# Performance work log

Measured on AMD Instinct MI355X. Metric: run time of the kernel, lower is better.

Reference implementation:

```python
import jax, jax.numpy as jnp
import numpy as np

N, E, IN_DIM, HID, OUT = 50000, 800000, 128, 128, 64


def setup_inputs() -> dict:
    key = jax.random.key(0)
    k = jax.random.split(key, 6)
    h = jax.random.normal(k[0], (N, IN_DIM), dtype=jnp.float32)
    edge_index = jax.random.randint(k[1], (2, E), 0, N, dtype=jnp.int64)
    s_in, s_hid = 1.0 / np.sqrt(IN_DIM), 1.0 / np.sqrt(HID)
    W_gcn = jax.random.uniform(k[2], (IN_DIM, HID), jnp.float32, -s_in, s_in)
    b_gcn = jnp.zeros((HID,), jnp.float32)
    W_fc = jax.random.uniform(k[3], (HID, OUT), jnp.float32, -s_hid, s_hid)
    b_fc = jax.random.uniform(k[4], (OUT,), jnp.float32, -s_hid, s_hid)
    return {"h": h, "edge_index": edge_index, "W_gcn": W_gcn,
            "b_gcn": b_gcn, "W_fc": W_fc, "b_fc": b_fc}


def reference(h, edge_index, W_gcn, b_gcn, W_fc, b_fc):
    n = h.shape[0]
    # GCNConv: transform, add self-loops, symmetric normalization, scatter-add
    x = h @ W_gcn                                   # [N, HID]
    loop = jnp.arange(n, dtype=edge_index.dtype)
    row = jnp.concatenate([edge_index[0], loop])    # source nodes
    col = jnp.concatenate([edge_index[1], loop])    # destination nodes
    deg = jax.ops.segment_sum(jnp.ones_like(col, dtype=x.dtype), col,
                              num_segments=n)       # in-degree incl. self-loop
    dinv = jnp.where(deg > 0, jax.lax.rsqrt(deg), 0.0)
    norm = dinv[row] * dinv[col]                    # [E+N]
    msg = x[row] * norm[:, None]                    # gather + scale
    agg = jax.ops.segment_sum(msg, col, num_segments=n) + b_gcn
    # ReLU then projection
    return jax.nn.relu(agg) @ W_fc + b_fc
```

## Files before the change

kernel.cpp:

```cpp
#include <hip/hip_runtime.h>

#define N_NODES 50000
#define N_EDGES 800000
#define TOT (N_EDGES + N_NODES)
#define NBKT 196
#define BCAP 6144

typedef __attribute__((ext_vector_type(4))) float floatx4;
typedef __attribute__((ext_vector_type(8))) _Float16 half8;
typedef __attribute__((ext_vector_type(2))) _Float16 half2v;

#define O_PTR   0UL
#define O_GF    200192UL
#define O_DINV  201472UL
#define O_ESRC  401664UL
#define O_W1    3801856UL
#define O_W2    3834624UL
#define O_U     3851008UL
#define O_H16   16651008UL

__global__ __launch_bounds__(256) void k_binA(const int* __restrict__ ei,
                                              int* __restrict__ gfill,
                                              unsigned* __restrict__ staging) {
    __shared__ int cnt[NBKT];
    __shared__ int gbase[NBKT];
    __shared__ int s_i64;
    int t = threadIdx.x;
    if (t < 64) {
        unsigned w = ((const unsigned*)ei)[2 * t + 1];
        unsigned long long m = __ballot(w == 0u);
        if (t == 0) s_i64 = (__popcll(m) >= 60) ? 1 : 0;
    }
    for (int i = t; i < NBKT; i += 256) cnt[i] = 0;
    __syncthreads();
    bool i64 = s_i64 != 0;
    int ebase = blockIdx.x * 4096;
    unsigned pk[16]; int rk[16]; short bk[16];
#pragma unroll
    for (int j = 0; j < 16; ++j) {
        int e = ebase + j * 256 + t;
        if (e < N_EDGES) {
            int s, d;
            if (i64) { s = ei[2 * e]; d = ei[2 * (N_EDGES + e)]; }
            else     { s = ei[e];     d = ei[N_EDGES + e]; }
            int b = d >> 8;
            bk[j] = (short)b;
            pk[j] = (unsigned)s | ((unsigned)(d & 255) << 16);
            rk[j] = atomicAdd(&cnt[b], 1);
        } else bk[j] = -1;
    }
    __syncthreads();
    for (int i = t; i < NBKT; i += 256)
        gbase[i] = atomicAdd(&gfill[i], cnt[i]);
    __syncthreads();
#pragma unroll
    for (int j = 0; j < 16; ++j) {
        if (bk[j] >= 0) {
            int pos = gbase[bk[j]] + rk[j];
            if (pos < BCAP) staging[(size_t)bk[j] * BCAP + pos] = pk[j];
        }
    }
}

__global__ __launch_bounds__(256) void k_binB(const unsigned* __restrict__ staging,
                                              const int* __restrict__ gfill,
                                              const float* __restrict__ h,
                                              const float* __restrict__ Wg,
                                              const float* __restrict__ Wf,
                                              int* __restrict__ ptr,
                                              float* __restrict__ dinv,
                                              _Float16* __restrict__ h16,
                                              _Float16* __restrict__ W1,
                                              _Float16* __restrict__ W2,
                                              int* __restrict__ esrc) {
    __shared__ unsigned se[BCAP];
    __shared__ int lcnt[256];
    __shared__ int lscan[256];
    __shared__ int cur[256];
    __shared__ float sdinv[256];
    __shared__ int s_cb;
    int b = blockIdx.x, t = threadIdx.x;
    if (b < 64) {
        int i = b * 256 + t;
        int n = i >> 7, k = i & 127;
        W1[i] = (_Float16)Wg[k * 128 + n];
    } else if (b < 96) {
        int i = (b - 64) * 256 + t;
        int n = i >> 7, k = i & 127;
        W2[i] = (_Float16)Wf[k * 64 + n];
    }
    int nbase = b * 256;
    int nn = min(256, N_NODES - nbase);
    int cnt = min(gfill[b], BCAP);
    if (t < 64) {
        int acc = 0;
        for (int i = t; i < b; i += 64) acc += min(gfill[i], BCAP) + 256;
#pragma unroll
        for (int off = 32; off > 0; off >>= 1) acc += __shfl_down(acc, off);
        if (t == 0) s_cb = acc;
    }
    lcnt[t] = 0;
    __syncthreads();
    int cb = s_cb;
    const unsigned* st = staging + (size_t)b * BCAP;
    for (int i = t; i < cnt; i += 256) {
        unsigned p = st[i];
        se[i] = p;
        atomicAdd(&lcnt[p >> 16], 1);
    }
    __syncthreads();
    int v = lcnt[t];
    lscan[t] = v;
    __syncthreads();
    for (int off = 1; off < 256; off <<= 1) {
        int x = (t >= off) ? lscan[t - off] : 0;
        __syncthreads(); lscan[t] += x; __syncthreads();
    }
    int segstart = cb + (lscan[t] - v) + t;
    float dv = rsqrtf((float)(v + 1));
    if (t < nn) {
        int node = nbase + t;
        ptr[node] = segstart;
        dinv[node] = dv;
        sdinv[t] = dv;
        esrc[segstart] = node;
        cur[t] = segstart + 1;
    }
    __syncthreads();
    for (int i = t; i < cnt; i += 256) {
        unsigned p = se[i];
        int pos = atomicAdd(&cur[p >> 16], 1);
        esrc[pos] = (int)(p & 0xffffu);
    }
    int half = t >> 7;
    int col = t & 127;
    for (int r = half; r < nn; r += 2) {
        int node = nbase + r;
        h16[(size_t)node * 128 + col] = (_Float16)(h[(size_t)node * 128 + col] * sdinv[r]);
    }
}

__global__ __launch_bounds__(256) void k_agg(const _Float16* __restrict__ h16,
                                             const int* __restrict__ ptr,
                                             const int* __restrict__ esrc,
                                             const float* __restrict__ dinv,
                                             _Float16* __restrict__ u) {
    int wid = (blockIdx.x * 256 + threadIdx.x) >> 6;
    int lane = threadIdx.x & 63;
    if (wid >= N_NODES) return;
    int p0 = ptr[wid];
    int p1 = (wid + 1 < N_NODES) ? ptr[wid + 1] : TOT;
    float a0 = 0.f, a1 = 0.f;
    for (int base = p0; base < p1; base += 64) {
        int cnt = p1 - base; if (cnt > 64) cnt = 64;
        int idx = 0;
        if (lane < cnt) idx = esrc[base + lane];
        int j = 0;
        for (; j + 8 <= cnt; j += 8) {
            int s0 = __shfl(idx, j),     s1 = __shfl(idx, j + 1);
            int s2 = __shfl(idx, j + 2), s3 = __shfl(idx, j + 3);
            int s4 = __shfl(idx, j + 4), s5 = __shfl(idx, j + 5);
            int s6 = __shfl(idx, j + 6), s7 = __shfl(idx, j + 7);
            half2v u0 = *(const half2v*)(h16 + (size_t)s0 * 128 + lane * 2);
            half2v u1 = *(const half2v*)(h16 + (size_t)s1 * 128 + lane * 2);
            half2v u2 = *(const half2v*)(h16 + (size_t)s2 * 128 + lane * 2);
            half2v u3 = *(const half2v*)(h16 + (size_t)s3 * 128 + lane * 2);
            half2v u4 = *(const half2v*)(h16 + (size_t)s4 * 128 + lane * 2);
            half2v u5 = *(const half2v*)(h16 + (size_t)s5 * 128 + lane * 2);
            half2v u6 = *(const half2v*)(h16 + (size_t)s6 * 128 + lane * 2);
            half2v u7 = *(const half2v*)(h16 + (size_t)s7 * 128 + lane * 2);
            a0 += (float)u0[0] + (float)u1[0] + (float)u2[0] + (float)u3[0]
                + (float)u4[0] + (float)u5[0] + (float)u6[0] + (float)u7[0];
            a1 += (float)u0[1] + (float)u1[1] + (float)u2[1] + (float)u3[1]
                + (float)u4[1] + (float)u5[1] + (float)u6[1] + (float)u7[1];
        }
        for (; j + 4 <= cnt; j += 4) {
            int s0 = __shfl(idx, j),     s1 = __shfl(idx, j + 1);
            int s2 = __shfl(idx, j + 2), s3 = __shfl(idx, j + 3);
            half2v u0 = *(const half2v*)(h16 + (size_t)s0 * 128 + lane * 2);
            half2v u1 = *(const half2v*)(h16 + (size_t)s1 * 128 + lane * 2);
            half2v u2 = *(const half2v*)(h16 + (size_t)s2 * 128 + lane * 2);
            half2v u3 = *(const half2v*)(h16 + (size_t)s3 * 128 + lane * 2);
            a0 += (float)u0[0] + (float)u1[0] + (float)u2[0] + (float)u3[0];
            a1 += (float)u0[1] + (float)u1[1] + (float)u2[1] + (float)u3[1];
        }
        for (; j < cnt; ++j) {
            int s = __shfl(idx, j);
            half2v uu = *(const half2v*)(h16 + (size_t)s * 128 + lane * 2);
            a0 += (float)uu[0]; a1 += (float)uu[1];
        }
    }
    float sc = dinv[wid];
    half2v o; o[0] = (_Float16)(a0 * sc); o[1] = (_Float16)(a1 * sc);
    *(half2v*)(u + (size_t)wid * 128 + lane * 2) = o;
}

__global__ __launch_bounds__(256) void k_gemmF(const _Float16* __restrict__ u,
                                               const _Float16* __restrict__ W1,
                                               const _Float16* __restrict__ W2,
                                               const float* __restrict__ bg,
                                               const float* __restrict__ bfc,
                                               float* __restrict__ out) {
    __shared__ _Float16 zt[4][16 * 128];
    int wave = threadIdx.x >> 6;
    int lane = threadIdx.x & 63;
    int rowbase = (blockIdx.x * 4 + wave) * 16;
    if (rowbase > N_NODES - 16) rowbase = N_NODES - 16;
    int quad = lane >> 4;
    int l15 = lane & 15;
    int mr = rowbase + l15;
    half8 a[4];
#pragma unroll
    for (int kk = 0; kk < 4; ++kk)
        a[kk] = *(const half8*)(u + (size_t)mr * 128 + kk * 32 + quad * 8);
    _Float16* z = zt[wave];
#pragma unroll
    for (int nt = 0; nt < 8; ++nt) {
        floatx4 acc = {0.f, 0.f, 0.f, 0.f};
        int n = nt * 16 + l15;
#pragma unroll
        for (int kk = 0; kk < 4; ++kk) {
            half8 bb = *(const half8*)(W1 + n * 128 + kk * 32 + quad * 8);
            acc = __builtin_amdgcn_mfma_f32_16x16x32_f16(a[kk], bb, acc, 0, 0, 0);
        }
        float bias = bg[n];
#pragma unroll
        for (int i = 0; i < 4; ++i) {
            int row = quad * 4 + i;
            z[row * 128 + n] = (_Float16)fmaxf(acc[i] + bias, 0.f);
        }
    }
    __syncthreads();
    half8 a2[4];
#pragma unroll
    for (int kk = 0; kk < 4; ++kk)
        a2[kk] = *(const half8*)(z + l15 * 128 + kk * 32 + quad * 8);
#pragma unroll
    for (int mt = 0; mt < 4; ++mt) {
        floatx4 acc = {0.f, 0.f, 0.f, 0.f};
        int n = mt * 16 + l15;
#pragma unroll
        for (int kk = 0; kk < 4; ++kk) {
            half8 bb = *(const half8*)(W2 + n * 128 + kk * 32 + quad * 8);
            acc = __builtin_amdgcn_mfma_f32_16x16x32_f16(a2[kk], bb, acc, 0, 0, 0);
        }
        float bias = bfc[n];
#pragma unroll
        for (int i = 0; i < 4; ++i) {
            int row = rowbase + quad * 4 + i;
            out[(size_t)row * 64 + n] = acc[i] + bias;
        }
    }
}

extern "C" void kernel_launch(void* const* d_in, const int* in_sizes, int n_in,
                              void* d_out, int out_size, void* d_ws, size_t ws_size,
                              hipStream_t stream) {
    (void)in_sizes; (void)n_in; (void)out_size; (void)ws_size;
    const float* h  = (const float*)d_in[0];
    const int*   ei = (const int*)d_in[1];
    const float* Wg = (const float*)d_in[2];
    const float* bg = (const float*)d_in[3];
    const float* Wf = (const float*)d_in[4];
    const float* bf = (const float*)d_in[5];
    float* out = (float*)d_out;

    char* ws = (char*)d_ws;
    int*      ptr   = (int*)(ws + O_PTR);
    int*      gfill = (int*)(ws + O_GF);
    float*    dinv  = (float*)(ws + O_DINV);
    int*      esrc  = (int*)(ws + O_ESRC);
    _Float16* W1    = (_Float16*)(ws + O_W1);
    _Float16* W2    = (_Float16*)(ws + O_W2);
    _Float16* u     = (_Float16*)(ws + O_U);
    _Float16* h16   = (_Float16*)(ws + O_H16);
    unsigned* staging = (unsigned*)(ws + O_U);

    hipMemsetAsync(gfill, 0, NBKT * sizeof(int), stream);
    k_binA<<<NBKT, 256, 0, stream>>>(ei, gfill, staging);
    k_binB<<<NBKT, 256, 0, stream>>>(staging, gfill, h, Wg, Wf,
                                     ptr, dinv, h16, W1, W2, esrc);
    k_agg<<<(N_NODES + 3) / 4, 256, 0, stream>>>(h16, ptr, esrc, dinv, u);
    k_gemmF<<<(N_NODES + 63) / 64, 256, 0, stream>>>(u, W1, W2, bg, bf, out);
}
```

Baseline: 176.5 us.

## Fuse aggregation with both GEMMs and vectorize edge-index loads in binning

The aggregation kernel and the two-layer MFMA GEMM kernel become one kernel. Each 256-thread block aggregates 16 nodes into shared memory and then runs both matmuls from there, so the fp16 intermediate no longer makes a round trip through global memory and one launch disappears. Self-loops are no longer stored as CSR entries; each node's own row is used to seed its accumulator. The binning kernel now reads edge indices with int4 vector loads of 16 contiguous edges per thread, which changes the access pattern. The risks are less parallelism in the aggregation phase, since each wave now handles 4 nodes serially, and each block's GEMM stalls on its slowest node.

```diff
diff --git a/kernel.cpp b/kernel.cpp
--- a/kernel.cpp
+++ b/kernel.cpp
@@ -2,7 +2,6 @@
 
 #define N_NODES 50000
 #define N_EDGES 800000
-#define TOT (N_EDGES + N_NODES)
 #define NBKT 196
 #define BCAP 6144
 
@@ -16,7 +15,7 @@
 #define O_ESRC  401664UL
 #define O_W1    3801856UL
 #define O_W2    3834624UL
-#define O_U     3851008UL
+#define O_STG   3851008UL
 #define O_H16   16651008UL
 
 __global__ __launch_bounds__(256) void k_binA(const int* __restrict__ ei,
@@ -34,18 +33,39 @@
     for (int i = t; i < NBKT; i += 256) cnt[i] = 0;
     __syncthreads();
     bool i64 = s_i64 != 0;
-    int ebase = blockIdx.x * 4096;
+    int e0 = blockIdx.x * 4096 + t * 16;
+    int sv[16], dvv[16];
+    if (i64) {
+        const int4* ps = (const int4*)(ei) + (e0 >> 1);
+        const int4* pd = (const int4*)(ei + 2 * (size_t)N_EDGES) + (e0 >> 1);
+#pragma unroll
+        for (int g = 0; g < 8; ++g) {
+            if (e0 + 2 * g < N_EDGES) {
+                int4 s4 = ps[g], d4 = pd[g];
+                sv[2 * g] = s4.x; sv[2 * g + 1] = s4.z;
+                dvv[2 * g] = d4.x; dvv[2 * g + 1] = d4.z;
+            } else { dvv[2 * g] = -1; dvv[2 * g + 1] = -1; }
+        }
+    } else {
+        const int4* ps = (const int4*)(ei) + (e0 >> 2);
+        const int4* pd = (const int4*)(ei + (size_t)N_EDGES) + (e0 >> 2);
+#pragma unroll
+        for (int g = 0; g < 4; ++g) {
+            if (e0 + 4 * g < N_EDGES) {
+                int4 s4 = ps[g], d4 = pd[g];
+                sv[4 * g] = s4.x; sv[4 * g + 1] = s4.y; sv[4 * g + 2] = s4.z; sv[4 * g + 3] = s4.w;
+                dvv[4 * g] = d4.x; dvv[4 * g + 1] = d4.y; dvv[4 * g + 2] = d4.z; dvv[4 * g + 3] = d4.w;
+            } else { dvv[4 * g] = -1; dvv[4 * g + 1] = -1; dvv[4 * g + 2] = -1; dvv[4 * g + 3] = -1; }
+        }
+    }
     unsigned pk[16]; int rk[16]; short bk[16];
 #pragma unroll
     for (int j = 0; j < 16; ++j) {
-        int e = ebase + j * 256 + t;
-        if (e < N_EDGES) {
-            int s, d;
-            if (i64) { s = ei[2 * e]; d = ei[2 * (N_EDGES + e)]; }
-            else     { s = ei[e];     d = ei[N_EDGES + e]; }
+        int d = dvv[j];
+        if (d >= 0 && e0 + j < N_EDGES) {
             int b = d >> 8;
             bk[j] = (short)b;
-            pk[j] = (unsigned)s | ((unsigned)(d & 255) << 16);
+            pk[j] = (unsigned)sv[j] | ((unsigned)(d & 255) << 16);
             rk[j] = atomicAdd(&cnt[b], 1);
         } else bk[j] = -1;
     }
@@ -94,7 +114,7 @@
     int cnt = min(gfill[b], BCAP);
     if (t < 64) {
         int acc = 0;
-        for (int i = t; i < b; i += 64) acc += min(gfill[i], BCAP) + 256;
+        for (int i = t; i < b; i += 64) acc += min(gfill[i], BCAP);
 #pragma unroll
         for (int off = 32; off > 0; off >>= 1) acc += __shfl_down(acc, off);
         if (t == 0) s_cb = acc;
@@ -116,15 +136,14 @@
         int x = (t >= off) ? lscan[t - off] : 0;
         __syncthreads(); lscan[t] += x; __syncthreads();
     }
-    int segstart = cb + (lscan[t] - v) + t;
+    int segstart = cb + (lscan[t] - v);
     float dv = rsqrtf((float)(v + 1));
     if (t < nn) {
         int node = nbase + t;
         ptr[node] = segstart;
         dinv[node] = dv;
         sdinv[t] = dv;
-        esrc[segstart] = node;
-        cur[t] = segstart + 1;
+        cur[t] = segstart;
     }
     __syncthreads();
     for (int i = t; i < cnt; i += 256) {
@@ -140,84 +159,80 @@
     }
 }
 
-__global__ __launch_bounds__(256) void k_agg(const _Float16* __restrict__ h16,
-                                             const int* __restrict__ ptr,
-                                             const int* __restrict__ esrc,
-                                             const float* __restrict__ dinv,
-                                             _Float16* __restrict__ u) {
-    int wid = (blockIdx.x * 256 + threadIdx.x) >> 6;
-    int lane = threadIdx.x & 63;
-    if (wid >= N_NODES) return;
-    int p0 = ptr[wid];
-    int p1 = (wid + 1 < N_NODES) ? ptr[wid + 1] : TOT;
-    float a0 = 0.f, a1 = 0.f;
-    for (int base = p0; base < p1; base += 64) {
-        int cnt = p1 - base; if (cnt > 64) cnt = 64;
-        int idx = 0;
-        if (lane < cnt) idx = esrc[base + lane];
-        int j = 0;
-        for (; j + 8 <= cnt; j += 8) {
-            int s0 = __shfl(idx, j),     s1 = __shfl(idx, j + 1);
-            int s2 = __shfl(idx, j + 2), s3 = __shfl(idx, j + 3);
-            int s4 = __shfl(idx, j + 4), s5 = __shfl(idx, j + 5);
-            int s6 = __shfl(idx, j + 6), s7 = __shfl(idx, j + 7);
-            half2v u0 = *(const half2v*)(h16 + (size_t)s0 * 128 + lane * 2);
-            half2v u1 = *(const half2v*)(h16 + (size_t)s1 * 128 + lane * 2);
-            half2v u2 = *(const half2v*)(h16 + (size_t)s2 * 128 + lane * 2);
-            half2v u3 = *(const half2v*)(h16 + (size_t)s3 * 128 + lane * 2);
-            half2v u4 = *(const half2v*)(h16 + (size_t)s4 * 128 + lane * 2);
-            half2v u5 = *(const half2v*)(h16 + (size_t)s5 * 128 + lane * 2);
-            half2v u6 = *(const half2v*)(h16 + (size_t)s6 * 128 + lane * 2);
-            half2v u7 = *(const half2v*)(h16 + (size_t)s7 * 128 + lane * 2);
-            a0 += (float)u0[0] + (float)u1[0] + (float)u2[0] + (float)u3[0]
-                + (float)u4[0] + (float)u5[0] + (float)u6[0] + (float)u7[0];
-            a1 += (float)u0[1] + (float)u1[1] + (float)u2[1] + (float)u3[1]
-                + (float)u4[1] + (float)u5[1] + (float)u6[1] + (float)u7[1];
-        }
-        for (; j + 4 <= cnt; j += 4) {
-            int s0 = __shfl(idx, j),     s1 = __shfl(idx, j + 1);
-            int s2 = __shfl(idx, j + 2), s3 = __shfl(idx, j + 3);
-            half2v u0 = *(const half2v*)(h16 + (size_t)s0 * 128 + lane * 2);
-            half2v u1 = *(const half2v*)(h16 + (size_t)s1 * 128 + lane * 2);
-            half2v u2 = *(const half2v*)(h16 + (size_t)s2 * 128 + lane * 2);
-            half2v u3 = *(const half2v*)(h16 + (size_t)s3 * 128 + lane * 2);
-            a0 += (float)u0[0] + (float)u1[0] + (float)u2[0] + (float)u3[0];
-            a1 += (float)u0[1] + (float)u1[1] + (float)u2[1] + (float)u3[1];
-        }
-        for (; j < cnt; ++j) {
-            int s = __shfl(idx, j);
-            half2v uu = *(const half2v*)(h16 + (size_t)s * 128 + lane * 2);
-            a0 += (float)uu[0]; a1 += (float)uu[1];
-        }
-    }
-    float sc = dinv[wid];
-    half2v o; o[0] = (_Float16)(a0 * sc); o[1] = (_Float16)(a1 * sc);
-    *(half2v*)(u + (size_t)wid * 128 + lane * 2) = o;
-}
-
-__global__ __launch_bounds__(256) void k_gemmF(const _Float16* __restrict__ u,
-                                               const _Float16* __restrict__ W1,
-                                               const _Float16* __restrict__ W2,
-                                               const float* __restrict__ bg,
-                                               const float* __restrict__ bfc,
-                                               float* __restrict__ out) {
-    __shared__ _Float16 zt[4][16 * 128];
+__global__ __launch_bounds__(256) void k_aggF(const _Float16* __restrict__ h16,
+                                              const int* __restrict__ ptr,
+                                              const int* __restrict__ esrc,
+                                              const float* __restrict__ dinv,
+                                              const _Float16* __restrict__ W1,
+                                              const _Float16* __restrict__ W2,
+                                              const float* __restrict__ bg,
+                                              const float* __restrict__ bfc,
+                                              float* __restrict__ out) {
+    __shared__ _Float16 ut[16 * 128];
+    __shared__ _Float16 z[16 * 128];
     int wave = threadIdx.x >> 6;
     int lane = threadIdx.x & 63;
-    int rowbase = (blockIdx.x * 4 + wave) * 16;
-    if (rowbase > N_NODES - 16) rowbase = N_NODES - 16;
-    int quad = lane >> 4;
-    int l15 = lane & 15;
-    int mr = rowbase + l15;
+    int nb = blockIdx.x * 16;
+    for (int q = 0; q < 4; ++q) {
+        int node = nb + wave * 4 + q;
+        int p0 = ptr[node];
+        int p1 = (node + 1 < N_NODES) ? ptr[node + 1] : N_EDGES;
+        half2v us = *(const half2v*)(h16 + (size_t)node * 128 + lane * 2);
+        float a0 = (float)us[0], a1 = (float)us[1];
+        for (int base = p0; base < p1; base += 64) {
+            int cnt = p1 - base; if (cnt > 64) cnt = 64;
+            int idx = 0;
+            if (lane < cnt) idx = esrc[base + lane];
+            int j = 0;
+            for (; j + 8 <= cnt; j += 8) {
+                int s0 = __shfl(idx, j),     s1 = __shfl(idx, j + 1);
+                int s2 = __shfl(idx, j + 2), s3 = __shfl(idx, j + 3);
+                int s4 = __shfl(idx, j + 4), s5 = __shfl(idx, j + 5);
+                int s6 = __shfl(idx, j + 6), s7 = __shfl(idx, j + 7);
+                half2v u0 = *(const half2v*)(h16 + (size_t)s0 * 128 + lane * 2);
+                half2v u1 = *(const half2v*)(h16 + (size_t)s1 * 128 + lane * 2);
+                half2v u2 = *(const half2v*)(h16 + (size_t)s2 * 128 + lane * 2);
+                half2v u3 = *(const half2v*)(h16 + (size_t)s3 * 128 + lane * 2);
+                half2v u4 = *(const half2v*)(h16 + (size_t)s4 * 128 + lane * 2);
+                half2v u5 = *(const half2v*)(h16 + (size_t)s5 * 128 + lane * 2);
+                half2v u6 = *(const half2v*)(h16 + (size_t)s6 * 128 + lane * 2);
+                half2v u7 = *(const half2v*)(h16 + (size_t)s7 * 128 + lane * 2);
+                a0 += (float)u0[0] + (float)u1[0] + (float)u2[0] + (float)u3[0]
+                    + (float)u4[0] + (float)u5[0] + (float)u6[0] + (float)u7[0];
+                a1 += (float)u0[1] + (float)u1[1] + (float)u2[1] + (float)u3[1]
+                    + (float)u4[1] + (float)u5[1] + (float)u6[1] + (float)u7[1];
+            }
+            for (; j + 4 <= cnt; j += 4) {
+                int s0 = __shfl(idx, j),     s1 = __shfl(idx, j + 1);
+                int s2 = __shfl(idx, j + 2), s3 = __shfl(idx, j + 3);
+                half2v u0 = *(const half2v*)(h16 + (size_t)s0 * 128 + lane * 2);
+                half2v u1 = *(const half2v*)(h16 + (size_t)s1 * 128 + lane * 2);
+                half2v u2 = *(const half2v*)(h16 + (size_t)s2 * 128 + lane * 2);
+                half2v u3 = *(const half2v*)(h16 + (size_t)s3 * 128 + lane * 2);
+                a0 += (float)u0[0] + (float)u1[0] + (float)u2[0] + (float)u3[0];
+                a1 += (float)u0[1] + (float)u1[1] + (float)u2[1] + (float)u3[1];
+            }
+            for (; j < cnt; ++j) {
+                int s = __shfl(idx, j);
+                half2v uu = *(const half2v*)(h16 + (size_t)s * 128 + lane * 2);
+                a0 += (float)uu[0]; a1 += (float)uu[1];
+            }
+        }
+        float sc = dinv[node];
+        int r = wave * 4 + q;
+        ut[r * 128 + lane * 2]     = (_Float16)(a0 * sc);
+        ut[r * 128 + lane * 2 + 1] = (_Float16)(a1 * sc);
+    }
+    __syncthreads();
+    int quad = lane >> 4, l15 = lane & 15;
     half8 a[4];
 #pragma unroll
     for (int kk = 0; kk < 4; ++kk)
-        a[kk] = *(const half8*)(u + (size_t)mr * 128 + kk * 32 + quad * 8);
-    _Float16* z = zt[wave];
-#pragma unroll
-    for (int nt = 0; nt < 8; ++nt) {
+        a[kk] = *(const half8*)(ut + l15 * 128 + kk * 32 + quad * 8);
+#pragma unroll
+    for (int tt = 0; tt < 2; ++tt) {
         floatx4 acc = {0.f, 0.f, 0.f, 0.f};
-        int n = nt * 16 + l15;
+        int n = (wave * 2 + tt) * 16 + l15;
 #pragma unroll
         for (int kk = 0; kk < 4; ++kk) {
             half8 bb = *(const half8*)(W1 + n * 128 + kk * 32 + quad * 8);
@@ -225,20 +240,17 @@
         }
         float bias = bg[n];
 #pragma unroll
-        for (int i = 0; i < 4; ++i) {
-            int row = quad * 4 + i;
-            z[row * 128 + n] = (_Float16)fmaxf(acc[i] + bias, 0.f);
-        }
+        for (int i = 0; i < 4; ++i)
+            z[(quad * 4 + i) * 128 + n] = (_Float16)fmaxf(acc[i] + bias, 0.f);
     }
     __syncthreads();
     half8 a2[4];
 #pragma unroll
     for (int kk = 0; kk < 4; ++kk)
         a2[kk] = *(const half8*)(z + l15 * 128 + kk * 32 + quad * 8);
-#pragma unroll
-    for (int mt = 0; mt < 4; ++mt) {
+    {
         floatx4 acc = {0.f, 0.f, 0.f, 0.f};
-        int n = mt * 16 + l15;
+        int n = wave * 16 + l15;
 #pragma unroll
         for (int kk = 0; kk < 4; ++kk) {
             half8 bb = *(const half8*)(W2 + n * 128 + kk * 32 + quad * 8);
@@ -246,10 +258,8 @@
         }
         float bias = bfc[n];
 #pragma unroll
-        for (int i = 0; i < 4; ++i) {
-            int row = rowbase + quad * 4 + i;
-            out[(size_t)row * 64 + n] = acc[i] + bias;
-        }
+        for (int i = 0; i < 4; ++i)
+            out[(size_t)(nb + quad * 4 + i) * 64 + n] = acc[i] + bias;
     }
 }
 
@@ -272,14 +282,13 @@
     int*      esrc  = (int*)(ws + O_ESRC);
     _Float16* W1    = (_Float16*)(ws + O_W1);
     _Float16* W2    = (_Float16*)(ws + O_W2);
-    _Float16* u     = (_Float16*)(ws + O_U);
+    unsigned* staging = (unsigned*)(ws + O_STG);
     _Float16* h16   = (_Float16*)(ws + O_H16);
-    unsigned* staging = (unsigned*)(ws + O_U);
 
     hipMemsetAsync(gfill, 0, NBKT * sizeof(int), stream);
     k_binA<<<NBKT, 256, 0, stream>>>(ei, gfill, staging);
     k_binB<<<NBKT, 256, 0, stream>>>(staging, gfill, h, Wg, Wf,
                                      ptr, dinv, h16, W1, W2, esrc);
-    k_agg<<<(N_NODES + 3) / 4, 256, 0, stream>>>(h16, ptr, esrc, dinv, u);
-    k_gemmF<<<(N_NODES + 63) / 64, 256, 0, stream>>>(u, W1, W2, bg, bf, out);
-}
+    k_aggF<<<N_NODES / 16, 256, 0, stream>>>(h16, ptr, esrc, dinv,
+                                             W1, W2, bg, bf, out);
+}
```

Result: faster. 155.1 us (-12.1%).
